# Kernel tuning notes

Hardware: AMD Instinct MI355X
Metric: run time of the kernel (lower is better)

The kernel has to match this reference:

```python
import math
import jax, jax.numpy as jnp
import numpy as np

E = 1024
H = 16
HD = E // H
MLP = 4 * E
EPS = 1e-6


def setup_inputs() -> dict:
    key = jax.random.key(0)
    ks = jax.random.split(key, 12)
    s = lambda fan_in: 1.0 / math.sqrt(fan_in)
    return {
        "x": jax.random.normal(ks[0], (8, 1024, E), dtype=jnp.float32),
        "ln1_g": jnp.ones((E,), jnp.float32),
        "ln1_b": jnp.zeros((E,), jnp.float32),
        "w_qkv": jax.random.normal(ks[1], (E, 3 * E), jnp.float32) * s(E),
        "b_qkv": jnp.zeros((3 * E,), jnp.float32),
        "w_o": jax.random.normal(ks[2], (E, E), jnp.float32) * s(E),
        "b_o": jnp.zeros((E,), jnp.float32),
        "ln2_g": jnp.ones((E,), jnp.float32),
        "ln2_b": jnp.zeros((E,), jnp.float32),
        "w_fc1": jax.random.normal(ks[3], (E, MLP), jnp.float32) * s(E),
        "b_fc1": jnp.zeros((MLP,), jnp.float32),
        "w_fc2": jax.random.normal(ks[4], (MLP, E), jnp.float32) * s(MLP),
        "b_fc2": jnp.zeros((E,), jnp.float32),
    }


def _layernorm(x, g, b):
    mu = jnp.mean(x, axis=-1, keepdims=True)
    var = jnp.mean(jnp.square(x - mu), axis=-1, keepdims=True)
    return (x - mu) * jax.lax.rsqrt(var + EPS) * g + b


def _attn(x, w_qkv, b_qkv, w_o, b_o):
    B, N, _ = x.shape
    qkv = (x @ w_qkv + b_qkv).reshape(B, N, 3, H, HD)
    q, k, v = qkv[:, :, 0], qkv[:, :, 1], qkv[:, :, 2]  # [B,N,H,HD]
    scores = jnp.einsum("bnhd,bmhd->bhnm", q, k) / math.sqrt(HD)
    probs = jax.nn.softmax(scores, axis=-1)
    out = jnp.einsum("bhnm,bmhd->bnhd", probs, v).reshape(B, N, H * HD)
    return out @ w_o + b_o


def reference(x, ln1_g, ln1_b, w_qkv, b_qkv, w_o, b_o, ln2_g, ln2_b,
              w_fc1, b_fc1, w_fc2, b_fc2):
    # pre-LN attention block with residual
    x = x + _attn(_layernorm(x, ln1_g, ln1_b), w_qkv, b_qkv, w_o, b_o)
    # pre-LN MLP block with residual (exact GELU, matching torch nn.GELU)
    h = _layernorm(x, ln2_g, ln2_b) @ w_fc1 + b_fc1
    h = jax.nn.gelu(h, approximate=False)
    x = x + (h @ w_fc2 + b_fc2)
    return x
```

## Files before the change

kernel.cpp:

```cpp
#include <hip/hip_runtime.h>
#include <stdint.h>

typedef unsigned short u16;
typedef __bf16 bf16x8 __attribute__((ext_vector_type(8)));
typedef float f32x4 __attribute__((ext_vector_type(4)));

#define GLD16(gp, lp) __builtin_amdgcn_global_load_lds( \
    (__attribute__((address_space(1))) void*)(uintptr_t)(gp), \
    (__attribute__((address_space(3))) void*)(uintptr_t)(lp), 16, 0, 0)

__device__ __forceinline__ u16 f2bf(float f) {
  uint32_t u = __builtin_bit_cast(uint32_t, f);
  u += 0x7FFFu + ((u >> 16) & 1u);
  return (u16)(u >> 16);
}

__global__ __launch_bounds__(256) void wtrans(const float* __restrict__ w,
                                              u16* __restrict__ wt, int K, int Nn) {
  __shared__ float tile[64][68];
  const int c0 = blockIdx.x << 6, r0 = blockIdx.y << 6;
  const int t = threadIdx.x, tr = t >> 2, tc = t & 3;
#pragma unroll
  for (int p = 0; p < 4; ++p) {
    float4 v = *(const float4*)&w[(size_t)(r0 + tr) * Nn + c0 + tc * 4 + p * 16];
    tile[tr][tc * 4 + p * 16 + 0] = v.x;
    tile[tr][tc * 4 + p * 16 + 1] = v.y;
    tile[tr][tc * 4 + p * 16 + 2] = v.z;
    tile[tr][tc * 4 + p * 16 + 3] = v.w;
  }
  __syncthreads();
#pragma unroll
  for (int p = 0; p < 4; ++p) {
    u16 e0 = f2bf(tile[tc * 4 + p * 16 + 0][tr]);
    u16 e1 = f2bf(tile[tc * 4 + p * 16 + 1][tr]);
    u16 e2 = f2bf(tile[tc * 4 + p * 16 + 2][tr]);
    u16 e3 = f2bf(tile[tc * 4 + p * 16 + 3][tr]);
    uint2 o;
    o.x = (uint32_t)e0 | ((uint32_t)e1 << 16);
    o.y = (uint32_t)e2 | ((uint32_t)e3 << 16);
    *(uint2*)&wt[(size_t)(c0 + tr) * K + r0 + tc * 4 + p * 16] = o;
  }
}

__global__ __launch_bounds__(256) void lnorm(const float* x, const float* __restrict__ g,
                                             const float* __restrict__ bta,
                                             u16* __restrict__ out) {
  const int lane = threadIdx.x & 63, wid = threadIdx.x >> 6;
  const size_t token = (size_t)blockIdx.x * 4 + wid;
  const float* row = x + token * 1024;
  float v[16];
#pragma unroll
  for (int i = 0; i < 4; ++i) {
    float4 f = *(const float4*)&row[(lane + i * 64) * 4];
    v[i * 4 + 0] = f.x; v[i * 4 + 1] = f.y; v[i * 4 + 2] = f.z; v[i * 4 + 3] = f.w;
  }
  float s = 0.f, s2 = 0.f;
#pragma unroll
  for (int i = 0; i < 16; ++i) { s += v[i]; s2 += v[i] * v[i]; }
  for (int off = 1; off < 64; off <<= 1) {
    s += __shfl_xor(s, off);
    s2 += __shfl_xor(s2, off);
  }
  const float mu = s * (1.0f / 1024.0f);
  const float var = s2 * (1.0f / 1024.0f) - mu * mu;
  const float rstd = rsqrtf(var + 1e-6f);
  u16* orow = out + token * 1024;
#pragma unroll
  for (int i = 0; i < 4; ++i) {
    const int c = (lane + i * 64) * 4;
    float4 gv = *(const float4*)&g[c];
    float4 bv = *(const float4*)&bta[c];
    u16 e0 = f2bf((v[i * 4 + 0] - mu) * rstd * gv.x + bv.x);
    u16 e1 = f2bf((v[i * 4 + 1] - mu) * rstd * gv.y + bv.y);
    u16 e2 = f2bf((v[i * 4 + 2] - mu) * rstd * gv.z + bv.z);
    u16 e3 = f2bf((v[i * 4 + 3] - mu) * rstd * gv.w + bv.w);
    uint2 o;
    o.x = (uint32_t)e0 | ((uint32_t)e1 << 16);
    o.y = (uint32_t)e2 | ((uint32_t)e3 << 16);
    *(uint2*)&orow[c] = o;
  }
}

template <int EPI>
__global__ __launch_bounds__(256) void gemm128(const u16* __restrict__ A,
                                               const u16* __restrict__ Bt,
                                               const float* __restrict__ bias,
                                               const float* res, void* Cout,
                                               int Ndim, int K, float qscale, int qlimit) {
  __shared__ __align__(16) u16 ldsA[2][4096];
  __shared__ __align__(16) u16 ldsB[2][4096];
  const int tid = threadIdx.x;
  const int lane = tid & 63;
  const int wid = tid >> 6;
  const int wm = wid & 1, wn = wid >> 1;
  const int m0 = blockIdx.y << 7, n0 = blockIdx.x << 7;

  const int srow = lane >> 2;
  const int slc = (lane & 3) ^ ((srow ^ (srow >> 2)) & 3);
  const u16* Ag = A + (size_t)(m0 + 32 * wid + srow) * K + slc * 8;
  const u16* Bg = Bt + (size_t)(n0 + 32 * wid + srow) * K + slc * 8;
  const size_t rstep = (size_t)16 * K;

  const int rrow = lane & 15;
  const int rc = ((lane >> 4) ^ ((rrow ^ (rrow >> 2)) & 3)) * 16;

  const f32x4 fzero = {0.f, 0.f, 0.f, 0.f};
  f32x4 acc[4][4];
#pragma unroll
  for (int i = 0; i < 4; ++i)
#pragma unroll
    for (int j = 0; j < 4; ++j) acc[i][j] = fzero;

  const int nk = K >> 5;
  GLD16(Ag, &ldsA[0][(2 * wid + 0) * 512]);
  GLD16(Ag + rstep, &ldsA[0][(2 * wid + 1) * 512]);
  GLD16(Bg, &ldsB[0][(2 * wid + 0) * 512]);
  GLD16(Bg + rstep, &ldsB[0][(2 * wid + 1) * 512]);
  __syncthreads();
  for (int kt = 0; kt < nk; ++kt) {
    const int cur = kt & 1;
    if (kt + 1 < nk) {
      const u16* a = Ag + (size_t)(kt + 1) * 32;
      const u16* b = Bg + (size_t)(kt + 1) * 32;
      GLD16(a, &ldsA[cur ^ 1][(2 * wid + 0) * 512]);
      GLD16(a + rstep, &ldsA[cur ^ 1][(2 * wid + 1) * 512]);
      GLD16(b, &ldsB[cur ^ 1][(2 * wid + 0) * 512]);
      GLD16(b + rstep, &ldsB[cur ^ 1][(2 * wid + 1) * 512]);
    }
    bf16x8 af[4], bfr[4];
#pragma unroll
    for (int mf = 0; mf < 4; ++mf)
      af[mf] = *(const bf16x8*)((const char*)&ldsA[cur][0] +
                                (wm * 64 + mf * 16 + rrow) * 64 + rc);
#pragma unroll
    for (int nf = 0; nf < 4; ++nf)
      bfr[nf] = *(const bf16x8*)((const char*)&ldsB[cur][0] +
                                 (wn * 64 + nf * 16 + rrow) * 64 + rc);
#pragma unroll
    for (int mf = 0; mf < 4; ++mf)
#pragma unroll
      for (int nf = 0; nf < 4; ++nf)
        acc[mf][nf] =
            __builtin_amdgcn_mfma_f32_16x16x32_bf16(af[mf], bfr[nf], acc[mf][nf], 0, 0, 0);
    __syncthreads();
  }
  const int g4 = (lane >> 4) << 2;
  const float cs = (EPI == 0 && n0 < qlimit) ? qscale : 1.0f;
#pragma unroll
  for (int nf = 0; nf < 4; ++nf) {
    const int col = n0 + wn * 64 + nf * 16 + rrow;
    const float bv = bias[col];
#pragma unroll
    for (int mf = 0; mf < 4; ++mf) {
#pragma unroll
      for (int r = 0; r < 4; ++r) {
        const int row = m0 + wm * 64 + mf * 16 + g4 + r;
        float v = acc[mf][nf][r] + bv;
        if (EPI == 0) v *= cs;
        if (EPI == 1) v = 0.5f * v * (1.0f + erff(v * 0.70710678118654752f));
        if (EPI == 2) {
          v += res[(size_t)row * Ndim + col];
          ((float*)Cout)[(size_t)row * Ndim + col] = v;
        } else {
          ((u16*)Cout)[(size_t)row * Ndim + col] = f2bf(v);
        }
      }
    }
  }
}

__global__ __launch_bounds__(256) void vtrans(const u16* __restrict__ qkv,
                                              u16* __restrict__ vt) {
  const int bh = blockIdx.y, b = bh >> 4, h = bh & 15;
  const int n0 = blockIdx.x << 6;
  __shared__ __align__(16) u16 tile[64][72];
  const int t = threadIdx.x, r = t >> 2, c = t & 3;
  const u16* src = qkv + (size_t)((b << 10) + n0 + r) * 3072 + 2048 + (h << 6);
#pragma unroll
  for (int p = 0; p < 2; ++p)
    *(uint4*)&tile[r][(c * 2 + p) * 8] = *(const uint4*)(src + (c * 2 + p) * 8);
  __syncthreads();
  u16* dst = vt + (size_t)((bh << 6) + r) * 1024 + n0;
#pragma unroll
  for (int p = 0; p < 2; ++p) {
    u16 o[8];
#pragma unroll
    for (int j = 0; j < 8; ++j) o[j] = tile[(c * 2 + p) * 8 + j][r];
    uint4 w;
    w.x = (uint32_t)o[0] | ((uint32_t)o[1] << 16);
    w.y = (uint32_t)o[2] | ((uint32_t)o[3] << 16);
    w.z = (uint32_t)o[4] | ((uint32_t)o[5] << 16);
    w.w = (uint32_t)o[6] | ((uint32_t)o[7] << 16);
    *(uint4*)&dst[(c * 2 + p) * 8] = w;
  }
}

__global__ __launch_bounds__(256) void attn64(const u16* __restrict__ qkv,
                                              const u16* __restrict__ vt,
                                              u16* __restrict__ aout) {
  const int bh = blockIdx.y, b = bh >> 4, h = bh & 15;
  const int q0 = blockIdx.x << 6;
  const int tid = threadIdx.x, lane = tid & 63, wid = tid >> 6;
  __shared__ __align__(16) u16 kl[4096];
  __shared__ __align__(16) u16 vl[4096];
  __shared__ __align__(16) u16 pl[4][1152];

  const int rrow = lane & 15;
  const int g = lane >> 4;
  const u16* qrow = qkv + (size_t)((b << 10) + q0 + (wid << 4) + rrow) * 3072 + (h << 6);
  bf16x8 qf0 = *(const bf16x8*)(qrow + (g << 3));
  bf16x8 qf1 = *(const bf16x8*)(qrow + 32 + (g << 3));

  const int sr = lane >> 3;
  const int lc = (lane & 7) ^ sr;
  const u16* kbase = qkv + (size_t)(b << 10) * 3072 + 1024 + (h << 6) +
                     (size_t)(16 * wid + sr) * 3072 + lc * 8;
  const u16* vbase = vt + (size_t)(bh << 6) * 1024 + (size_t)(16 * wid + sr) * 1024 + lc * 8;

  const f32x4 fzero = {0.f, 0.f, 0.f, 0.f};
  f32x4 oacc[4];
#pragma unroll
  for (int i = 0; i < 4; ++i) oacc[i] = fzero;
  f32x4 lacc = fzero;
  const int rcb = lane & 7;
  u16* plw = &pl[wid][0];

  for (int t = 0; t < 16; ++t) {
    const int kt0 = t << 6;
    GLD16(kbase + (size_t)kt0 * 3072, &kl[(2 * wid + 0) * 512]);
    GLD16(kbase + (size_t)kt0 * 3072 + 8 * 3072, &kl[(2 * wid + 1) * 512]);
    GLD16(vbase + kt0, &vl[(2 * wid + 0) * 512]);
    GLD16(vbase + kt0 + 8 * 1024, &vl[(2 * wid + 1) * 512]);
    __syncthreads();

    f32x4 s4[4];
#pragma unroll
    for (int i = 0; i < 4; ++i) s4[i] = fzero;
#pragma unroll
    for (int nf = 0; nf < 4; ++nf) {
      bf16x8 k0 = *(const bf16x8*)((const char*)kl + (nf * 16 + rrow) * 128 +
                                   ((g + 0) ^ rcb) * 16);
      bf16x8 k1 = *(const bf16x8*)((const char*)kl + (nf * 16 + rrow) * 128 +
                                   ((g + 4) ^ rcb) * 16);
      s4[nf] = __builtin_amdgcn_mfma_f32_16x16x32_bf16(k0, qf0, s4[nf], 0, 0, 0);
      s4[nf] = __builtin_amdgcn_mfma_f32_16x16x32_bf16(k1, qf1, s4[nf], 0, 0, 0);
    }

#pragma unroll
    for (int nf = 0; nf < 4; ++nf) {
      float p0 = exp2f(s4[nf][0]);
      float p1 = exp2f(s4[nf][1]);
      float p2 = exp2f(s4[nf][2]);
      float p3 = exp2f(s4[nf][3]);
      f32x4 pv = {p0, p1, p2, p3};
      lacc += pv;
      uint32_t a0 = __builtin_bit_cast(uint32_t, p0) + 0x8000u;
      uint32_t a1 = __builtin_bit_cast(uint32_t, p1) + 0x8000u;
      uint32_t a2 = __builtin_bit_cast(uint32_t, p2) + 0x8000u;
      uint32_t a3 = __builtin_bit_cast(uint32_t, p3) + 0x8000u;
      uint2 w;
      w.x = __builtin_amdgcn_perm(a1, a0, 0x07060302);
      w.y = __builtin_amdgcn_perm(a3, a2, 0x07060302);
      *(uint2*)(plw + rrow * 72 + nf * 16 + (g << 2)) = w;
    }

    bf16x8 pf0 = *(const bf16x8*)((const char*)plw + rrow * 144 + (g << 4));
    bf16x8 pf1 = *(const bf16x8*)((const char*)plw + rrow * 144 + (g << 4) + 64);
#pragma unroll
    for (int nf = 0; nf < 4; ++nf) {
      bf16x8 v0 = *(const bf16x8*)((const char*)vl + (nf * 16 + rrow) * 128 +
                                   ((g + 0) ^ rcb) * 16);
      bf16x8 v1 = *(const bf16x8*)((const char*)vl + (nf * 16 + rrow) * 128 +
                                   ((g + 4) ^ rcb) * 16);
      oacc[nf] = __builtin_amdgcn_mfma_f32_16x16x32_bf16(pf0, v0, oacc[nf], 0, 0, 0);
      oacc[nf] = __builtin_amdgcn_mfma_f32_16x16x32_bf16(pf1, v1, oacc[nf], 0, 0, 0);
    }
    __syncthreads();
  }

  float lsum = lacc[0] + lacc[1] + lacc[2] + lacc[3];
  lsum += __shfl_xor(lsum, 16);
  lsum += __shfl_xor(lsum, 32);
  const float inv = 1.0f / lsum;
  float invq[4];
#pragma unroll
  for (int r = 0; r < 4; ++r) {
    int bi = __builtin_amdgcn_ds_bpermute(((g << 2) + r) << 2,
                                          __builtin_bit_cast(int, inv));
    invq[r] = __builtin_bit_cast(float, bi);
  }
  u16* ob = aout + (size_t)((b << 10) + q0 + (wid << 4)) * 1024 + (h << 6);
#pragma unroll
  for (int nf = 0; nf < 4; ++nf)
#pragma unroll
    for (int r = 0; r < 4; ++r)
      ob[(size_t)(g * 4 + r) * 1024 + nf * 16 + rrow] = f2bf(oacc[nf][r] * invq[r]);
}

extern "C" void kernel_launch(void* const* d_in, const int* in_sizes, int n_in,
                              void* d_out, int out_size, void* d_ws, size_t ws_size,
                              hipStream_t stream) {
  const float* x = (const float*)d_in[0];
  const float* ln1_g = (const float*)d_in[1];
  const float* ln1_b = (const float*)d_in[2];
  const float* w_qkv = (const float*)d_in[3];
  const float* b_qkv = (const float*)d_in[4];
  const float* w_o = (const float*)d_in[5];
  const float* b_o = (const float*)d_in[6];
  const float* ln2_g = (const float*)d_in[7];
  const float* ln2_b = (const float*)d_in[8];
  const float* w_fc1 = (const float*)d_in[9];
  const float* b_fc1 = (const float*)d_in[10];
  const float* w_fc2 = (const float*)d_in[11];
  const float* b_fc2 = (const float*)d_in[12];
  float* out = (float*)d_out;

  char* w = (char*)d_ws;
  u16* wqkvT = (u16*)w; w += (size_t)3072 * 1024 * 2;
  u16* woT   = (u16*)w; w += (size_t)1024 * 1024 * 2;
  u16* wfc1T = (u16*)w; w += (size_t)4096 * 1024 * 2;
  u16* wfc2T = (u16*)w; w += (size_t)1024 * 4096 * 2;
  u16* xn    = (u16*)w; w += (size_t)8192 * 1024 * 2;
  u16* qkvb  = (u16*)w; w += (size_t)8192 * 3072 * 2;
  u16* vtb   = (u16*)w; w += (size_t)128 * 64 * 1024 * 2;
  u16* attnb = (u16*)w; w += (size_t)8192 * 1024 * 2;
  u16* hbuf  = qkvb;

  const float QS = 0.18033688011112042f;

  wtrans<<<dim3(48, 16), 256, 0, stream>>>(w_qkv, wqkvT, 1024, 3072);
  wtrans<<<dim3(16, 16), 256, 0, stream>>>(w_o, woT, 1024, 1024);
  wtrans<<<dim3(64, 16), 256, 0, stream>>>(w_fc1, wfc1T, 1024, 4096);
  wtrans<<<dim3(16, 64), 256, 0, stream>>>(w_fc2, wfc2T, 4096, 1024);

  lnorm<<<2048, 256, 0, stream>>>(x, ln1_g, ln1_b, xn);
  gemm128<0><<<dim3(24, 64), 256, 0, stream>>>(xn, wqkvT, b_qkv, nullptr, qkvb, 3072, 1024, QS, 1024);
  vtrans<<<dim3(16, 128), 256, 0, stream>>>(qkvb, vtb);
  attn64<<<dim3(16, 128), 256, 0, stream>>>(qkvb, vtb, attnb);
  gemm128<2><<<dim3(8, 64), 256, 0, stream>>>(attnb, woT, b_o, x, out, 1024, 1024, 1.f, 0);
  lnorm<<<2048, 256, 0, stream>>>(out, ln2_g, ln2_b, xn);
  gemm128<1><<<dim3(32, 64), 256, 0, stream>>>(xn, wfc1T, b_fc1, nullptr, hbuf, 4096, 1024, 1.f, 0);
  gemm128<2><<<dim3(8, 64), 256, 0, stream>>>(hbuf, wfc2T, b_fc2, out, out, 1024, 4096, 1.f, 0);
}
```

Before: 434.9 us.

## Swizzle GEMM block order across XCDs and simplify LDS staging layout

Measured after the change: 414.1 us. 4.8% less time.

```diff
diff --git a/kernel.cpp b/kernel.cpp
--- a/kernel.cpp
+++ b/kernel.cpp
@@ -8,6 +8,8 @@
 #define GLD16(gp, lp) __builtin_amdgcn_global_load_lds( \
     (__attribute__((address_space(1))) void*)(uintptr_t)(gp), \
     (__attribute__((address_space(3))) void*)(uintptr_t)(lp), 16, 0, 0)
+
+#define MM(a, b, c) __builtin_amdgcn_mfma_f32_16x16x32_bf16(a, b, c, 0, 0, 0)
 
 __device__ __forceinline__ u16 f2bf(float f) {
   uint32_t u = __builtin_bit_cast(uint32_t, f);
@@ -82,27 +84,32 @@
 }
 
 template <int EPI>
-__global__ __launch_bounds__(256) void gemm128(const u16* __restrict__ A,
-                                               const u16* __restrict__ Bt,
-                                               const float* __restrict__ bias,
-                                               const float* res, void* Cout,
-                                               int Ndim, int K, float qscale, int qlimit) {
-  __shared__ __align__(16) u16 ldsA[2][4096];
-  __shared__ __align__(16) u16 ldsB[2][4096];
-  const int tid = threadIdx.x;
-  const int lane = tid & 63;
-  const int wid = tid >> 6;
+__global__ __launch_bounds__(256, 4) void g97(const u16* __restrict__ A,
+                                              const u16* __restrict__ Bt,
+                                              const float* __restrict__ bias,
+                                              const float* res, void* Cout,
+                                              int Ndim, int K, float qscale,
+                                              int qlimit, int gn) {
+  __shared__ __align__(16) u16 lds[2][8192];
+  const int tid = threadIdx.x, lane = tid & 63, wid = tid >> 6;
   const int wm = wid & 1, wn = wid >> 1;
-  const int m0 = blockIdx.y << 7, n0 = blockIdx.x << 7;
-
-  const int srow = lane >> 2;
-  const int slc = (lane & 3) ^ ((srow ^ (srow >> 2)) & 3);
-  const u16* Ag = A + (size_t)(m0 + 32 * wid + srow) * K + slc * 8;
-  const u16* Bg = Bt + (size_t)(n0 + 32 * wid + srow) * K + slc * 8;
-  const size_t rstep = (size_t)16 * K;
-
-  const int rrow = lane & 15;
-  const int rc = ((lane >> 4) ^ ((rrow ^ (rrow >> 2)) & 3)) * 16;
+
+  const int wg = blockIdx.x;
+  const int swz = (wg & 7) * ((int)gridDim.x >> 3) + (wg >> 3);
+  const int mblk = swz / gn, nb = swz - mblk * gn;
+  const int m0 = mblk << 7, n0 = nb << 7;
+
+  const int srow = tid >> 2;
+  const int gsub = (tid & 3) ^ ((tid >> 3) & 3);
+  const u16* Ag = A + (size_t)(m0 + srow) * K + gsub * 8;
+  const u16* Bg = Bt + (size_t)(n0 + srow) * K + gsub * 8;
+  const size_t rstep = (size_t)64 * K;
+  char* lb = (char*)&lds[0][0];
+
+  const int rrow = lane & 15, g = lane >> 4;
+  const int xg = g ^ ((rrow >> 1) & 3);
+  const int aoff = (wm * 64 + rrow) * 64 + xg * 16;
+  const int boff = 8192 + (wn * 64 + rrow) * 64 + xg * 16;
 
   const f32x4 fzero = {0.f, 0.f, 0.f, 0.f};
   f32x4 acc[4][4];
@@ -111,52 +118,49 @@
 #pragma unroll
     for (int j = 0; j < 4; ++j) acc[i][j] = fzero;
 
+#define STG(kt, s) do { \
+    char* d_ = lb + (s) * 16384; \
+    GLD16(Ag + (size_t)(kt) * 32, d_ + tid * 16); \
+    GLD16(Ag + rstep + (size_t)(kt) * 32, d_ + 4096 + tid * 16); \
+    GLD16(Bg + (size_t)(kt) * 32, d_ + 8192 + tid * 16); \
+    GLD16(Bg + rstep + (size_t)(kt) * 32, d_ + 12288 + tid * 16); \
+  } while (0)
+
   const int nk = K >> 5;
-  GLD16(Ag, &ldsA[0][(2 * wid + 0) * 512]);
-  GLD16(Ag + rstep, &ldsA[0][(2 * wid + 1) * 512]);
-  GLD16(Bg, &ldsB[0][(2 * wid + 0) * 512]);
-  GLD16(Bg + rstep, &ldsB[0][(2 * wid + 1) * 512]);
+  STG(0, 0);
   __syncthreads();
   for (int kt = 0; kt < nk; ++kt) {
-    const int cur = kt & 1;
-    if (kt + 1 < nk) {
-      const u16* a = Ag + (size_t)(kt + 1) * 32;
-      const u16* b = Bg + (size_t)(kt + 1) * 32;
-      GLD16(a, &ldsA[cur ^ 1][(2 * wid + 0) * 512]);
-      GLD16(a + rstep, &ldsA[cur ^ 1][(2 * wid + 1) * 512]);
-      GLD16(b, &ldsB[cur ^ 1][(2 * wid + 0) * 512]);
-      GLD16(b + rstep, &ldsB[cur ^ 1][(2 * wid + 1) * 512]);
-    }
+    if (kt + 1 < nk) STG(kt + 1, (kt + 1) & 1);
+    const char* sb = lb + (kt & 1) * 16384;
     bf16x8 af[4], bfr[4];
 #pragma unroll
     for (int mf = 0; mf < 4; ++mf)
-      af[mf] = *(const bf16x8*)((const char*)&ldsA[cur][0] +
-                                (wm * 64 + mf * 16 + rrow) * 64 + rc);
+      af[mf] = *(const bf16x8*)(sb + aoff + mf * 1024);
 #pragma unroll
     for (int nf = 0; nf < 4; ++nf)
-      bfr[nf] = *(const bf16x8*)((const char*)&ldsB[cur][0] +
-                                 (wn * 64 + nf * 16 + rrow) * 64 + rc);
+      bfr[nf] = *(const bf16x8*)(sb + boff + nf * 1024);
 #pragma unroll
     for (int mf = 0; mf < 4; ++mf)
 #pragma unroll
       for (int nf = 0; nf < 4; ++nf)
-        acc[mf][nf] =
-            __builtin_amdgcn_mfma_f32_16x16x32_bf16(af[mf], bfr[nf], acc[mf][nf], 0, 0, 0);
+        acc[mf][nf] = MM(af[mf], bfr[nf], acc[mf][nf]);
     __syncthreads();
   }
+#undef STG
+
   const int g4 = (lane >> 4) << 2;
-  const float cs = (EPI == 0 && n0 < qlimit) ? qscale : 1.0f;
 #pragma unroll
   for (int nf = 0; nf < 4; ++nf) {
     const int col = n0 + wn * 64 + nf * 16 + rrow;
-    const float bv = bias[col];
+    const float bvb = bias[col];
+    const float csf = (EPI == 0 && col < qlimit) ? qscale : 1.0f;
 #pragma unroll
     for (int mf = 0; mf < 4; ++mf) {
 #pragma unroll
       for (int r = 0; r < 4; ++r) {
         const int row = m0 + wm * 64 + mf * 16 + g4 + r;
-        float v = acc[mf][nf][r] + bv;
-        if (EPI == 0) v *= cs;
+        float v = acc[mf][nf][r] + bvb;
+        if (EPI == 0) v *= csf;
         if (EPI == 1) v = 0.5f * v * (1.0f + erff(v * 0.70710678118654752f));
         if (EPI == 2) {
           v += res[(size_t)row * Ndim + col];
@@ -334,11 +338,11 @@
   wtrans<<<dim3(16, 64), 256, 0, stream>>>(w_fc2, wfc2T, 4096, 1024);
 
   lnorm<<<2048, 256, 0, stream>>>(x, ln1_g, ln1_b, xn);
-  gemm128<0><<<dim3(24, 64), 256, 0, stream>>>(xn, wqkvT, b_qkv, nullptr, qkvb, 3072, 1024, QS, 1024);
+  g97<0><<<1536, 256, 0, stream>>>(xn, wqkvT, b_qkv, nullptr, qkvb, 3072, 1024, QS, 1024, 24);
   vtrans<<<dim3(16, 128), 256, 0, stream>>>(qkvb, vtb);
   attn64<<<dim3(16, 128), 256, 0, stream>>>(qkvb, vtb, attnb);
-  gemm128<2><<<dim3(8, 64), 256, 0, stream>>>(attnb, woT, b_o, x, out, 1024, 1024, 1.f, 0);
+  g97<2><<<512, 256, 0, stream>>>(attnb, woT, b_o, x, out, 1024, 1024, 1.f, 0, 8);
   lnorm<<<2048, 256, 0, stream>>>(out, ln2_g, ln2_b, xn);
-  gemm128<1><<<dim3(32, 64), 256, 0, stream>>>(xn, wfc1T, b_fc1, nullptr, hbuf, 4096, 1024, 1.f, 0);
-  gemm128<2><<<dim3(8, 64), 256, 0, stream>>>(hbuf, wfc2T, b_fc2, out, out, 1024, 4096, 1.f, 0);
-}
+  g97<1><<<2048, 256, 0, stream>>>(xn, wfc1T, b_fc1, nullptr, hbuf, 4096, 1024, 1.f, 0, 32);
+  g97<2><<<512, 256, 0, stream>>>(hbuf, wfc2T, b_fc2, out, out, 1024, 4096, 1.f, 0, 8);
+}
```
